# Optimization experiments

Measured on AMD Instinct MI355X. Metric: run time of the kernel, lower is better.

The kernel has to match this reference:

```python
import math
import jax
import jax.numpy as jnp
import numpy as np
from jax import lax

B_, L, D_MODEL = 2, 1024, 2048
D_STATE, D_CONV, EXPAND = 16, 4, 2
D_INNER = EXPAND * D_MODEL          # 4096
DT_RANK = math.ceil(D_MODEL / 16)   # 128


def setup_inputs() -> dict:
    key = jax.random.key(0)
    ks = jax.random.split(key, 8)
    hidden_states = jax.random.normal(ks[0], (B_, L, D_MODEL), jnp.float32)
    in_proj_w = jax.random.normal(ks[1], (2 * D_INNER, D_MODEL), jnp.float32) * (D_MODEL ** -0.5)
    conv_w = jax.random.normal(ks[2], (D_INNER, D_CONV), jnp.float32) * (D_CONV ** -0.5)
    conv_b = jnp.zeros((D_INNER,), jnp.float32)
    x_proj_w = jax.random.normal(ks[3], (DT_RANK + 2 * D_STATE, D_INNER), jnp.float32) * (D_INNER ** -0.5)
    dt_std = DT_RANK ** -0.5
    dt_proj_w = jax.random.uniform(ks[4], (D_INNER, DT_RANK), jnp.float32, minval=-dt_std, maxval=dt_std)
    # dt bias init: softplus^{-1} of dt sampled log-uniform in [1e-3, 1e-1]
    dt = jnp.exp(jax.random.uniform(ks[5], (D_INNER,), jnp.float32)
                 * (math.log(0.1) - math.log(0.001)) + math.log(0.001))
    dt = jnp.clip(dt, 1e-4)
    dt_proj_b = dt + jnp.log(-jnp.expm1(-dt))
    A_log = jnp.log(jnp.broadcast_to(jnp.arange(1, D_STATE + 1, dtype=jnp.float32), (D_INNER, D_STATE)))
    D = jnp.ones((D_INNER,), jnp.float32)
    out_proj_w = jax.random.normal(ks[6], (D_MODEL, D_INNER), jnp.float32) * (D_INNER ** -0.5)
    return {
        'hidden_states': hidden_states, 'in_proj_w': in_proj_w,
        'conv_w': conv_w, 'conv_b': conv_b, 'x_proj_w': x_proj_w,
        'dt_proj_w': dt_proj_w, 'dt_proj_b': dt_proj_b,
        'A_log': A_log, 'D': D, 'out_proj_w': out_proj_w,
    }


def _silu(v):
    return v * jax.nn.sigmoid(v)


def _mamba_forward(hidden_states, in_proj_w, conv_w, conv_b, x_proj_w,
                   dt_proj_w, dt_proj_b, A_log, D, out_proj_w):
    b, l, _ = hidden_states.shape
    # in_proj: (b,l,d_model) -> (b, 2*d_inner, l)
    xz = jnp.einsum('bld,ed->bel', hidden_states, in_proj_w)
    x, z = xz[:, :D_INNER, :], xz[:, D_INNER:, :]
    A = -jnp.exp(A_log.astype(jnp.float32))  # (d_inner, d_state)
    # causal depthwise conv1d + SiLU
    xp = jnp.pad(x, ((0, 0), (0, 0), (D_CONV - 1, 0)))
    x = lax.conv_general_dilated(
        xp, conv_w[:, None, :], window_strides=(1,), padding='VALID',
        dimension_numbers=('NCH', 'OIH', 'NCH'), feature_group_count=D_INNER)
    x = _silu(x + conv_b[None, :, None])  # (b, d_inner, l)
    # x_proj -> dt, B, C
    x_dbl = jnp.einsum('bdl,kd->blk', x, x_proj_w)  # (b,l,dt_rank+2n)
    dt_lo = x_dbl[..., :DT_RANK]
    Bmat = x_dbl[..., DT_RANK:DT_RANK + D_STATE]          # (b,l,n)
    Cmat = x_dbl[..., DT_RANK + D_STATE:]                 # (b,l,n)
    delta = jax.nn.softplus(jnp.einsum('blr,dr->bld', dt_lo, dt_proj_w)
                            + dt_proj_b.astype(jnp.float32))  # (b,l,d)
    xt = jnp.transpose(x, (2, 0, 1))       # (l,b,d)
    dl = jnp.transpose(delta, (1, 0, 2))   # (l,b,d)
    Bl = jnp.transpose(Bmat, (1, 0, 2))    # (l,b,n)
    Cl = jnp.transpose(Cmat, (1, 0, 2))    # (l,b,n)

    def step(h, inp):
        d_t, B_t, C_t, x_t = inp
        dA = jnp.exp(d_t[..., None] * A)                       # (b,d,n)
        h = h * dA + d_t[..., None] * B_t[:, None, :] * x_t[..., None]
        y_t = jnp.sum(h * C_t[:, None, :], axis=-1)            # (b,d)
        return h, y_t

    h0 = jnp.zeros((b, D_INNER, D_STATE), jnp.float32)
    _, ys = lax.scan(step, h0, (dl, Bl, Cl, xt))  # ys: (l,b,d)
    y = jnp.transpose(ys, (1, 0, 2))              # (b,l,d)
    y = y + jnp.transpose(x, (0, 2, 1)) * D[None, None, :]
    y = y * _silu(jnp.transpose(z, (0, 2, 1)))
    out = jnp.einsum('bld,ed->ble', y, out_proj_w)  # (b,l,d_model)
    return out


def reference(hidden_states, in_proj_w, conv_w, conv_b, x_proj_w,
              dt_proj_w, dt_proj_b, A_log, D, out_proj_w):
    return _mamba_forward(hidden_states, in_proj_w, conv_w, conv_b, x_proj_w,
                          dt_proj_w, dt_proj_b, A_log, D, out_proj_w)
```

## Files before the change

### kernel.cpp

```cpp
#include <hip/hip_runtime.h>
#include <hip/hip_bf16.h>
#include <stdint.h>

#define BB 2
#define LL 1024
#define DMODEL 2048
#define DINNER 4096
#define DSTATE 16
#define DTRANK 128
#define XDBL_LD 256
#define CHUNK 64
#define NCH (LL / CHUNK)

typedef unsigned short ushort;
using short8 = __attribute__((ext_vector_type(8))) short;
using f32x4  = __attribute__((ext_vector_type(4))) float;
using us4    = __attribute__((ext_vector_type(4))) ushort;

__device__ __forceinline__ float bf2f(ushort u) {
    union { uint32_t i; float f; } v; v.i = ((uint32_t)u) << 16; return v.f;
}
__device__ __forceinline__ ushort f2bf(float f) {
    union { float f; uint32_t i; } v; v.f = f;
    uint32_t lsb = (v.i >> 16) & 1u;
    uint32_t r = v.i + 0x7FFFu + lsb;
    return (ushort)(r >> 16);
}

__device__ __forceinline__ void glds16(const ushort* g, ushort* l) {
    __builtin_amdgcn_global_load_lds(
        (const __attribute__((address_space(1))) void*)g,
        (__attribute__((address_space(3))) void*)l,
        16, 0, 0);
}

__global__ __launch_bounds__(256) void cvt_kernel(
    const float4* __restrict__ in, us4* __restrict__ out, int n4)
{
    int i = blockIdx.x * 256 + threadIdx.x;
    if (i < n4) {
        float4 v = in[i];
        us4 o;
        o.x = f2bf(v.x); o.y = f2bf(v.y); o.z = f2bf(v.z); o.w = f2bf(v.w);
        out[i] = o;
    }
}

__global__ __launch_bounds__(256) void pad_xproj(
    const float* __restrict__ w, ushort* __restrict__ wp)
{
    int gid = blockIdx.x * 256 + threadIdx.x;
    int r = gid >> 12;
    wp[gid] = (r < 160) ? f2bf(w[gid]) : (ushort)0;
}

template <int EPI, bool WF, bool WH>
__global__ __launch_bounds__(256) void gemm_nt(
    const ushort* __restrict__ A, int lda,
    const ushort* __restrict__ Bm, int ldb,
    float* __restrict__ Cf, ushort* __restrict__ Ch, int ldc,
    int K, const float* __restrict__ bias)
{
    __shared__ __align__(16) ushort sA[128 * 32];
    __shared__ __align__(16) ushort sB[128 * 32];

    const int tid  = threadIdx.x;
    const int lane = tid & 63;
    const int wave = tid >> 6;
    const int wr = wave >> 1, wc = wave & 1;
    const long m0 = (long)blockIdx.y * 128;
    const long n0 = (long)blockIdx.x * 128;

    const long zoff = (long)blockIdx.z;
    A  += zoff * (long)K;
    Bm += zoff * (long)K;
    const long Mrows = (long)gridDim.y * 128;
    if (WF) Cf += zoff * Mrows * (long)ldc;
    if (WH) Ch += zoff * Mrows * (long)ldc;

    f32x4 acc[4][4] = {};

    const int lrow = lane & 15;
    const int lko  = (lane >> 4) << 3;

    const int sr = tid >> 2;
    const int sc = (tid & 3) << 3;
    const ushort* Ag = A  + (m0 + sr) * (long)lda + sc;
    const ushort* Bg = Bm + (n0 + sr) * (long)ldb + sc;
    ushort* lA = sA + tid * 8;
    ushort* lB = sB + tid * 8;

    for (int k0 = 0; k0 < K; k0 += 32) {
        __syncthreads();
        glds16(Ag + k0, lA);
        glds16(Ag + 64 * (long)lda + k0, lA + 2048);
        glds16(Bg + k0, lB);
        glds16(Bg + 64 * (long)ldb + k0, lB + 2048);
        __syncthreads();

        short8 af[4], bf[4];
        #pragma unroll
        for (int i = 0; i < 4; ++i)
            af[i] = *(const short8*)&sA[(wr * 64 + i * 16 + lrow) * 32 + lko];
        #pragma unroll
        for (int j = 0; j < 4; ++j)
            bf[j] = *(const short8*)&sB[(wc * 64 + j * 16 + lrow) * 32 + lko];

        #pragma unroll
        for (int i = 0; i < 4; ++i)
            #pragma unroll
            for (int j = 0; j < 4; ++j)
                acc[i][j] = __builtin_amdgcn_mfma_f32_16x16x32_bf16(
                    af[i], bf[j], acc[i][j], 0, 0, 0);
    }

    const int r0 = (lane >> 4) * 4;
    const int c0 = lane & 15;
    #pragma unroll
    for (int i = 0; i < 4; ++i) {
        #pragma unroll
        for (int j = 0; j < 4; ++j) {
            long col = n0 + wc * 64 + j * 16 + c0;
            float bv = 0.f;
            if (EPI == 1) bv = bias[col];
            #pragma unroll
            for (int r = 0; r < 4; ++r) {
                long row = m0 + wr * 64 + i * 16 + r0 + r;
                float v = acc[i][j][r];
                if (EPI == 1) {
                    v += bv;
                    v = (v > 20.f) ? v : log1pf(__expf(v));
                }
                long idx = row * (long)ldc + col;
                if (WF) Cf[idx] = v;
                if (WH) Ch[idx] = f2bf(v);
            }
        }
    }
}

template <int NZ, bool WH_>
__global__ __launch_bounds__(256) void reduce_k(
    const float4* __restrict__ parts, long stride4, int n4,
    float4* __restrict__ outF, us4* __restrict__ outH)
{
    int i = blockIdx.x * 256 + threadIdx.x;
    if (i >= n4) return;
    float4 s = parts[i];
    #pragma unroll
    for (int z = 1; z < NZ; ++z) {
        float4 v = parts[(long)z * stride4 + i];
        s.x += v.x; s.y += v.y; s.z += v.z; s.w += v.w;
    }
    if (outF) outF[i] = s;
    if (WH_) {
        us4 o; o.x = f2bf(s.x); o.y = f2bf(s.y); o.z = f2bf(s.z); o.w = f2bf(s.w);
        outH[i] = o;
    }
}

__global__ __launch_bounds__(256) void conv_silu_kernel(
    const ushort* __restrict__ xz,
    const float* __restrict__ cw,
    const float* __restrict__ cb,
    ushort* __restrict__ xc)
{
    int gid = blockIdx.x * 256 + threadIdx.x;
    int d  = gid & (DINNER - 1);
    int rl = gid >> 12;
    int l  = rl & (LL - 1);
    float acc = cb[d];
    #pragma unroll
    for (int j = 0; j < 4; ++j) {
        int li = l - 3 + j;
        if (li >= 0)
            acc += cw[d * 4 + j] * bf2f(xz[(long)(rl - 3 + j) * 8192 + d]);
    }
    float s = acc / (1.f + __expf(-acc));
    xc[gid] = f2bf(s);
}

__global__ __launch_bounds__(256) void scan_p1(
    const ushort* __restrict__ delta,
    const ushort* __restrict__ xc,
    const float*  __restrict__ xdbl,
    const float*  __restrict__ A_log,
    float* __restrict__ Hbuf,
    float* __restrict__ sumdt_buf)
{
    __shared__ float sB[CHUNK * 16];
    const int tid = threadIdx.x;
    const int k = blockIdx.y, b = blockIdx.z;
    const int d = blockIdx.x * 256 + tid;
    const int row0 = b * LL + k * CHUNK;

    #pragma unroll
    for (int i = 0; i < 4; ++i) {
        int idx = i * 256 + tid;
        sB[idx] = xdbl[(long)(row0 + (idx >> 4)) * XDBL_LD + DTRANK + (idx & 15)];
    }
    __syncthreads();

    float A[DSTATE];
    const float4* Ap = (const float4*)(A_log + d * DSTATE);
    #pragma unroll
    for (int i = 0; i < 4; ++i) {
        float4 v = Ap[i];
        A[i*4+0] = -__expf(v.x); A[i*4+1] = -__expf(v.y);
        A[i*4+2] = -__expf(v.z); A[i*4+3] = -__expf(v.w);
    }

    float H[DSTATE];
    #pragma unroll
    for (int s = 0; s < DSTATE; ++s) H[s] = 0.f;
    float sumdt = 0.f;

    for (int t = 0; t < CHUNK; ++t) {
        const long row = row0 + t;
        const float dt = bf2f(delta[row * DINNER + d]);
        const float xv = bf2f(xc[row * DINNER + d]);
        const float dx = dt * xv;
        sumdt += dt;
        #pragma unroll
        for (int s = 0; s < DSTATE; ++s) {
            float dA = __expf(dt * A[s]);
            H[s] = H[s] * dA + dx * sB[t * 16 + s];
        }
    }

    const long o = ((long)(b * NCH + k) * DINNER + d) * DSTATE;
    float4* Ho = (float4*)(Hbuf + o);
    #pragma unroll
    for (int i = 0; i < 4; ++i) {
        float4 v; v.x = H[i*4+0]; v.y = H[i*4+1]; v.z = H[i*4+2]; v.w = H[i*4+3];
        Ho[i] = v;
    }
    sumdt_buf[(b * NCH + k) * DINNER + d] = sumdt;
}

__global__ __launch_bounds__(256) void scan_p2(
    const float* __restrict__ A_log,
    const float* __restrict__ sumdt_buf,
    float* __restrict__ Hbuf)
{
    int gid = blockIdx.x * 256 + threadIdx.x;
    int b = gid >> 16;
    int rem = gid & 65535;
    int d = rem >> 4, s = rem & 15;
    float A = -__expf(A_log[d * DSTATE + s]);
    float h = 0.f;
    for (int k = 0; k < NCH; ++k) {
        long idx = ((long)(b * NCH + k) * DINNER + d) * DSTATE + s;
        float Hk = Hbuf[idx];
        float sd = sumdt_buf[(b * NCH + k) * DINNER + d];
        Hbuf[idx] = h;
        h = h * __expf(A * sd) + Hk;
    }
}

__global__ __launch_bounds__(256) void scan_p3(
    const ushort* __restrict__ delta,
    const ushort* __restrict__ xc,
    const float*  __restrict__ xdbl,
    const ushort* __restrict__ xz,
    const float*  __restrict__ A_log,
    const float*  __restrict__ Dp,
    const float*  __restrict__ hin,
    ushort* __restrict__ y)
{
    __shared__ float sBC[CHUNK * 32];
    const int tid = threadIdx.x;
    const int k = blockIdx.y, b = blockIdx.z;
    const int d = blockIdx.x * 256 + tid;
    const int row0 = b * LL + k * CHUNK;

    #pragma unroll
    for (int i = 0; i < 8; ++i) {
        int idx = i * 256 + tid;
        sBC[idx] = xdbl[(long)(row0 + (idx >> 5)) * XDBL_LD + DTRANK + (idx & 31)];
    }
    __syncthreads();

    float A[DSTATE];
    const float4* Ap = (const float4*)(A_log + d * DSTATE);
    #pragma unroll
    for (int i = 0; i < 4; ++i) {
        float4 v = Ap[i];
        A[i*4+0] = -__expf(v.x); A[i*4+1] = -__expf(v.y);
        A[i*4+2] = -__expf(v.z); A[i*4+3] = -__expf(v.w);
    }
    const float Dd = Dp[d];

    float h[DSTATE];
    const float4* Hp = (const float4*)(hin + ((long)(b * NCH + k) * DINNER + d) * DSTATE);
    #pragma unroll
    for (int i = 0; i < 4; ++i) {
        float4 v = Hp[i];
        h[i*4+0] = v.x; h[i*4+1] = v.y; h[i*4+2] = v.z; h[i*4+3] = v.w;
    }

    for (int t = 0; t < CHUNK; ++t) {
        const long row = row0 + t;
        const float dt = bf2f(delta[row * DINNER + d]);
        const float xv = bf2f(xc[row * DINNER + d]);
        const float dx = dt * xv;
        float yt = 0.f;
        #pragma unroll
        for (int s = 0; s < DSTATE; ++s) {
            float dA = __expf(dt * A[s]);
            h[s] = h[s] * dA + dx * sBC[t * 32 + s];
            yt += h[s] * sBC[t * 32 + 16 + s];
        }
        yt += xv * Dd;
        const float zv = bf2f(xz[row * 8192 + DINNER + d]);
        yt *= zv / (1.f + __expf(-zv));
        y[row * DINNER + d] = f2bf(yt);
    }
}

extern "C" void kernel_launch(void* const* d_in, const int* in_sizes, int n_in,
                              void* d_out, int out_size, void* d_ws, size_t ws_size,
                              hipStream_t stream)
{
    const float* hidden    = (const float*)d_in[0];
    const float* in_proj   = (const float*)d_in[1];
    const float* conv_w    = (const float*)d_in[2];
    const float* conv_b    = (const float*)d_in[3];
    const float* x_proj    = (const float*)d_in[4];
    const float* dt_proj_w = (const float*)d_in[5];
    const float* dt_proj_b = (const float*)d_in[6];
    const float* A_log     = (const float*)d_in[7];
    const float* Dp        = (const float*)d_in[8];
    const float* out_proj  = (const float*)d_in[9];
    float* out = (float*)d_out;

    char* ws = (char*)d_ws;
    ushort* xz_h    = (ushort*)(ws);
    ushort* xc      = (ushort*)(ws + 33554432);
    ushort* xpp     = (ushort*)(ws + 50331648);
    float*  xdbl    = (float*)(ws + 52428800);
    ushort* xdblh   = (ushort*)(ws + 54525952);
    ushort* delta_h = (ushort*)(ws + 55574528);
    ushort* yb      = (ushort*)(ws + 72351744);
    ushort* hid_h   = (ushort*)(ws + 89128960);
    ushort* inp_h   = (ushort*)(ws + 97517568);
    float*  parts   = (float*)(ws + 97517568);
    float*  Hbuf    = (float*)(ws + 97517568);
    float*  sumdt   = (float*)(ws + 105906176);
    ushort* dtp_h   = (ushort*)(ws + 131072000);
    ushort* outp_h  = (ushort*)(ws + 132120576);

    const int M = BB * LL;

    cvt_kernel<<<(2048 * 2048) / 1024, 256, 0, stream>>>(
        (const float4*)hidden, (us4*)hid_h, (2048 * 2048) / 4);
    cvt_kernel<<<(8192 * 2048) / 1024, 256, 0, stream>>>(
        (const float4*)in_proj, (us4*)inp_h, (8192 * 2048) / 4);
    cvt_kernel<<<(4096 * 128) / 1024, 256, 0, stream>>>(
        (const float4*)dt_proj_w, (us4*)dtp_h, (4096 * 128) / 4);
    cvt_kernel<<<(2048 * 4096) / 1024, 256, 0, stream>>>(
        (const float4*)out_proj, (us4*)outp_h, (2048 * 4096) / 4);
    pad_xproj<<<(256 * 4096) / 256, 256, 0, stream>>>(x_proj, xpp);

    gemm_nt<0, false, true><<<dim3(8192 / 128, M / 128), 256, 0, stream>>>(
        hid_h, DMODEL, inp_h, DMODEL, nullptr, xz_h, 8192, DMODEL, nullptr);

    conv_silu_kernel<<<(M * DINNER) / 256, 256, 0, stream>>>(xz_h, conv_w, conv_b, xc);

    gemm_nt<0, true, false><<<dim3(XDBL_LD / 128, M / 128, 16), 256, 0, stream>>>(
        xc, DINNER, xpp, DINNER, parts, nullptr, XDBL_LD, DINNER / 16, nullptr);
    reduce_k<16, true><<<(M * XDBL_LD / 4 + 255) / 256, 256, 0, stream>>>(
        (const float4*)parts, (long)M * XDBL_LD / 4, M * XDBL_LD / 4,
        (float4*)xdbl, (us4*)xdblh);

    gemm_nt<1, false, true><<<dim3(DINNER / 128, M / 128), 256, 0, stream>>>(
        xdblh, XDBL_LD, dtp_h, DTRANK, nullptr, delta_h, DINNER, DTRANK, dt_proj_b);

    scan_p1<<<dim3(DINNER / 256, NCH, BB), 256, 0, stream>>>(
        delta_h, xc, xdbl, A_log, Hbuf, sumdt);
    scan_p2<<<(BB * DINNER * DSTATE) / 256, 256, 0, stream>>>(
        A_log, sumdt, Hbuf);
    scan_p3<<<dim3(DINNER / 256, NCH, BB), 256, 0, stream>>>(
        delta_h, xc, xdbl, xz_h, A_log, Dp, Hbuf, yb);

    gemm_nt<0, true, false><<<dim3(DMODEL / 128, M / 128, 2), 256, 0, stream>>>(
        yb, DINNER, outp_h, DINNER, parts, nullptr, DMODEL, DINNER / 2, nullptr);
    reduce_k<2, false><<<(M * DMODEL / 4 + 255) / 256, 256, 0, stream>>>(
        (const float4*)parts, (long)M * DMODEL / 4, M * DMODEL / 4,
        (float4*)out, nullptr);
}
```

Baseline: 517.0 us.

## Use 32x32 MFMA tiles, XCD-aware block remap, and fuse conversion kernels

The GEMM inner loop moves from 16x16x32 to 32x32x16 bf16 MFMA instructions with 2x2 accumulator tiles per wave, which cuts LDS fragment reads per MFMA. Block indices are remapped so that consecutive blocks, which the hardware spreads round-robin over the 8 XCDs, give each XCD a contiguous strip of N tiles for better L2 reuse. The five fp32-to-bf16 conversion and padding launches are merged into one kernel to cut launch overhead. The new epilogue row mapping must match the 32x32 accumulator layout, and the 2D remap only applies when the grid's N-tile count is a multiple of 8.

Measured after the change: 514.7 us. About the same (-0.4%).

```diff
diff --git a/kernel.cpp b/kernel.cpp
--- a/kernel.cpp
+++ b/kernel.cpp
@@ -14,7 +14,7 @@
 
 typedef unsigned short ushort;
 using short8 = __attribute__((ext_vector_type(8))) short;
-using f32x4  = __attribute__((ext_vector_type(4))) float;
+using f32x16 = __attribute__((ext_vector_type(16))) float;
 using us4    = __attribute__((ext_vector_type(4))) ushort;
 
 __device__ __forceinline__ float bf2f(ushort u) {
@@ -34,24 +34,27 @@
         16, 0, 0);
 }
 
-__global__ __launch_bounds__(256) void cvt_kernel(
-    const float4* __restrict__ in, us4* __restrict__ out, int n4)
-{
-    int i = blockIdx.x * 256 + threadIdx.x;
-    if (i < n4) {
-        float4 v = in[i];
-        us4 o;
-        o.x = f2bf(v.x); o.y = f2bf(v.y); o.z = f2bf(v.z); o.w = f2bf(v.w);
-        out[i] = o;
-    }
-}
-
-__global__ __launch_bounds__(256) void pad_xproj(
-    const float* __restrict__ w, ushort* __restrict__ wp)
-{
-    int gid = blockIdx.x * 256 + threadIdx.x;
-    int r = gid >> 12;
-    wp[gid] = (r < 160) ? f2bf(w[gid]) : (ushort)0;
+__global__ __launch_bounds__(256) void cvt_all(
+    const float4* __restrict__ hidden, const float4* __restrict__ inproj,
+    const float4* __restrict__ dtw, const float4* __restrict__ outp,
+    const float4* __restrict__ xproj,
+    us4* __restrict__ hid_h, us4* __restrict__ inp_h, us4* __restrict__ dtp_h,
+    us4* __restrict__ outp_h, us4* __restrict__ xpp)
+{
+    long i = (long)blockIdx.x * 256 + threadIdx.x;
+    const float4* src; us4* dst; long j;
+    if (i < 1048576)      { src = hidden; dst = hid_h;  j = i; }
+    else if (i < 5242880) { src = inproj; dst = inp_h;  j = i - 1048576; }
+    else if (i < 5373952) { src = dtw;    dst = dtp_h;  j = i - 5242880; }
+    else if (i < 7471104) { src = outp;   dst = outp_h; j = i - 5373952; }
+    else {
+        j = i - 7471104; dst = xpp;
+        if (j >= 163840) { us4 z = {0, 0, 0, 0}; dst[j] = z; return; }
+        src = xproj;
+    }
+    float4 v = src[j];
+    us4 o; o.x = f2bf(v.x); o.y = f2bf(v.y); o.z = f2bf(v.z); o.w = f2bf(v.w);
+    dst[j] = o;
 }
 
 template <int EPI, bool WF, bool WH>
@@ -68,20 +71,31 @@
     const int lane = tid & 63;
     const int wave = tid >> 6;
     const int wr = wave >> 1, wc = wave & 1;
-    const long m0 = (long)blockIdx.y * 128;
-    const long n0 = (long)blockIdx.x * 128;
+
+    const int NT = gridDim.x, MT = gridDim.y;
+    int mt, nt;
+    if ((NT & 7) == 0) {
+        int lin   = blockIdx.y * NT + blockIdx.x;
+        int strip = NT >> 3;
+        int xcd   = lin & 7;
+        int idx   = lin >> 3;
+        nt = xcd * strip + (idx % strip);
+        mt = idx / strip;
+    } else { mt = blockIdx.y; nt = blockIdx.x; }
+    const long m0 = (long)mt * 128;
+    const long n0 = (long)nt * 128;
 
     const long zoff = (long)blockIdx.z;
     A  += zoff * (long)K;
     Bm += zoff * (long)K;
-    const long Mrows = (long)gridDim.y * 128;
+    const long Mrows = (long)MT * 128;
     if (WF) Cf += zoff * Mrows * (long)ldc;
     if (WH) Ch += zoff * Mrows * (long)ldc;
 
-    f32x4 acc[4][4] = {};
-
-    const int lrow = lane & 15;
-    const int lko  = (lane >> 4) << 3;
+    f32x16 acc[2][2] = {};
+
+    const int l31 = lane & 31;
+    const int lhk = (lane >> 5) << 3;
 
     const int sr = tid >> 2;
     const int sc = (tid & 3) << 3;
@@ -98,35 +112,38 @@
         glds16(Bg + 64 * (long)ldb + k0, lB + 2048);
         __syncthreads();
 
-        short8 af[4], bf[4];
+        short8 af[2][2], bfr[2][2];
         #pragma unroll
-        for (int i = 0; i < 4; ++i)
-            af[i] = *(const short8*)&sA[(wr * 64 + i * 16 + lrow) * 32 + lko];
+        for (int i = 0; i < 2; ++i)
+            #pragma unroll
+            for (int ks = 0; ks < 2; ++ks) {
+                af[i][ks]  = *(const short8*)&sA[(wr * 64 + i * 32 + l31) * 32 + ks * 16 + lhk];
+                bfr[i][ks] = *(const short8*)&sB[(wc * 64 + i * 32 + l31) * 32 + ks * 16 + lhk];
+            }
+
         #pragma unroll
-        for (int j = 0; j < 4; ++j)
-            bf[j] = *(const short8*)&sB[(wc * 64 + j * 16 + lrow) * 32 + lko];
-
+        for (int ks = 0; ks < 2; ++ks)
+            #pragma unroll
+            for (int i = 0; i < 2; ++i)
+                #pragma unroll
+                for (int j = 0; j < 2; ++j)
+                    acc[i][j] = __builtin_amdgcn_mfma_f32_32x32x16_bf16(
+                        af[i][ks], bfr[j][ks], acc[i][j], 0, 0, 0);
+    }
+
+    const int rq = (lane >> 5) << 2;
+    #pragma unroll
+    for (int i = 0; i < 2; ++i) {
         #pragma unroll
-        for (int i = 0; i < 4; ++i)
-            #pragma unroll
-            for (int j = 0; j < 4; ++j)
-                acc[i][j] = __builtin_amdgcn_mfma_f32_16x16x32_bf16(
-                    af[i], bf[j], acc[i][j], 0, 0, 0);
-    }
-
-    const int r0 = (lane >> 4) * 4;
-    const int c0 = lane & 15;
-    #pragma unroll
-    for (int i = 0; i < 4; ++i) {
-        #pragma unroll
-        for (int j = 0; j < 4; ++j) {
-            long col = n0 + wc * 64 + j * 16 + c0;
+        for (int j = 0; j < 2; ++j) {
+            long col = n0 + wc * 64 + j * 32 + l31;
             float bv = 0.f;
             if (EPI == 1) bv = bias[col];
             #pragma unroll
-            for (int r = 0; r < 4; ++r) {
-                long row = m0 + wr * 64 + i * 16 + r0 + r;
-                float v = acc[i][j][r];
+            for (int reg = 0; reg < 16; ++reg) {
+                int rin = (reg & 3) + ((reg >> 2) << 3) + rq;
+                long row = m0 + wr * 64 + i * 32 + rin;
+                float v = acc[i][j][reg];
                 if (EPI == 1) {
                     v += bv;
                     v = (v > 20.f) ? v : log1pf(__expf(v));
@@ -352,15 +369,10 @@
 
     const int M = BB * LL;
 
-    cvt_kernel<<<(2048 * 2048) / 1024, 256, 0, stream>>>(
-        (const float4*)hidden, (us4*)hid_h, (2048 * 2048) / 4);
-    cvt_kernel<<<(8192 * 2048) / 1024, 256, 0, stream>>>(
-        (const float4*)in_proj, (us4*)inp_h, (8192 * 2048) / 4);
-    cvt_kernel<<<(4096 * 128) / 1024, 256, 0, stream>>>(
-        (const float4*)dt_proj_w, (us4*)dtp_h, (4096 * 128) / 4);
-    cvt_kernel<<<(2048 * 4096) / 1024, 256, 0, stream>>>(
-        (const float4*)out_proj, (us4*)outp_h, (2048 * 4096) / 4);
-    pad_xproj<<<(256 * 4096) / 256, 256, 0, stream>>>(x_proj, xpp);
+    cvt_all<<<30208, 256, 0, stream>>>(
+        (const float4*)hidden, (const float4*)in_proj, (const float4*)dt_proj_w,
+        (const float4*)out_proj, (const float4*)x_proj,
+        (us4*)hid_h, (us4*)inp_h, (us4*)dtp_h, (us4*)outp_h, (us4*)xpp);
 
     gemm_nt<0, false, true><<<dim3(8192 / 128, M / 128), 256, 0, stream>>>(
         hid_h, DMODEL, inp_h, DMODEL, nullptr, xz_h, 8192, DMODEL, nullptr);
```
